# Kernel tuning notes

Measured on AMD Instinct MI355X. Metric: run time of the kernel, lower is better.

Reference implementation:

```python
import jax, jax.numpy as jnp
import numpy as np

N, E, T, Q, G = 50000, 800000, 1000000, 1000000, 4096
L, H, D, HID, ED = 3, 8, 16, 128, 16
EPS = 1e-8


def setup_inputs() -> dict:
    key = jax.random.key(0)
    ks = jax.random.split(key, 20)
    inp = {
        "x": jax.random.normal(ks[0], (N, HID), jnp.float32),
        "pos": jax.random.normal(ks[1], (N, 3), jnp.float32),
        "edge_attr": jax.random.normal(ks[2], (E, ED), jnp.float32),
        "temps": jax.random.uniform(ks[3], (G, 1), jnp.float32),
        "edge_index": jax.random.randint(ks[4], (2, E), 0, N, jnp.int32),
        "triple_index": jax.random.randint(ks[5], (3, T), 0, N, jnp.int32),
        "quadra_index": jax.random.randint(ks[6], (4, Q), 0, N, jnp.int32),
        "batch": jnp.sort(jax.random.randint(ks[7], (N,), 0, G, jnp.int32)),
        "W": jax.random.normal(ks[8], (L, HID, HID), jnp.float32) * 0.08,
        "a_e": jax.random.normal(ks[9], (L, H, 2 * D + 1), jnp.float32) * 0.1,
        "a_t": jax.random.normal(ks[10], (L, H, 2 * D + 1), jnp.float32) * 0.1,
        "a_q": jax.random.normal(ks[11], (L, H, 2 * D + 1), jnp.float32) * 0.1,
        "We": jax.random.normal(ks[12], (L, ED, H), jnp.float32) * 0.1,
        "W1": jax.random.normal(ks[13], (2 * HID + 1, 256), jnp.float32) * 0.06,
        "b1": jnp.zeros((256,), jnp.float32),
        "W2": jax.random.normal(ks[14], (256, 256), jnp.float32) * 0.06,
        "b2": jnp.zeros((256,), jnp.float32),
        "W3": jax.random.normal(ks[15], (256, 1), jnp.float32) * 0.06,
        "b3": jnp.zeros((1,), jnp.float32),
    }
    return inp


def _seg_softmax(logits, seg, n):
    # numerically stable segment softmax over destination nodes
    m = jax.ops.segment_max(logits, seg, num_segments=n)
    m = jnp.where(jnp.isfinite(m), m, 0.0)
    e = jnp.exp(logits - m[seg])
    s = jax.ops.segment_sum(e, seg, num_segments=n)
    return e / (s[seg] + 1e-16)


def _hop(hh, src, dst, geom, a, bias=None):
    # hh: [N,H,D]; gather-attend-scatter for one interaction order
    q, k = hh[dst], hh[src]                      # [M,H,D]
    logits = jnp.einsum('mhd,hd->mh', q, a[:, :D]) \
           + jnp.einsum('mhd,hd->mh', k, a[:, D:2 * D]) \
           + geom[:, None] * a[:, 2 * D]
    if bias is not None:
        logits = logits + bias
    logits = jax.nn.leaky_relu(logits, 0.2)
    alpha = _seg_softmax(logits, dst, hh.shape[0])  # [M,H]
    return jax.ops.segment_sum(k * alpha[..., None], dst, num_segments=hh.shape[0])


def _geom_features(pos, edge_index, triple_index, quadra_index):
    # edge distance
    d = jnp.linalg.norm(pos[edge_index[0]] - pos[edge_index[1]] + EPS, axis=-1)
    # triple angle cos at center node j of (i,j,k)
    i, j, k = triple_index
    u, v = pos[i] - pos[j], pos[k] - pos[j]
    cos_a = (u * v).sum(-1) / (jnp.linalg.norm(u, axis=-1) * jnp.linalg.norm(v, axis=-1) + EPS)
    # quadra dihedral cos of (p0,p1,p2,p3)
    p0, p1, p2, p3 = pos[quadra_index[0]], pos[quadra_index[1]], pos[quadra_index[2]], pos[quadra_index[3]]
    b1, b2, b3 = p1 - p0, p2 - p1, p3 - p2
    n1, n2 = jnp.cross(b1, b2), jnp.cross(b2, b3)
    cos_d = (n1 * n2).sum(-1) / (jnp.linalg.norm(n1, axis=-1) * jnp.linalg.norm(n2, axis=-1) + EPS)
    return d, cos_a, cos_d


def reference(x, pos, edge_attr, temps, edge_index, triple_index, quadra_index, batch,
              W, a_e, a_t, a_q, We, W1, b1, W2, b2, W3, b3):
    d, cos_a, cos_d = _geom_features(pos, edge_index, triple_index, quadra_index)
    e_src, e_dst = edge_index[1], edge_index[0]
    t_src, t_dst = triple_index[2], triple_index[0]
    q_src, q_dst = quadra_index[3], quadra_index[0]
    h = x
    for l in range(L):
        hl = h @ W[l]                              # [N,HID]
        hh = hl.reshape(N, H, D)
        bias_e = edge_attr @ We[l]                 # [E,H]
        agg = _hop(hh, e_src, e_dst, d, a_e[l], bias_e) \
            + _hop(hh, t_src, t_dst, cos_a, a_t[l]) \
            + _hop(hh, q_src, q_dst, cos_d, a_q[l])
        h = jax.nn.elu(hl + agg.reshape(N, HID))
    # readout: sum + max pooling per graph, concat temperature scalar
    s = jax.ops.segment_sum(h, batch, num_segments=G)
    mx = jax.ops.segment_max(h, batch, num_segments=G)
    mx = jnp.where(jnp.isfinite(mx), mx, 0.0)
    mol = jnp.concatenate([s, mx, temps], axis=-1)  # [G, 2*HID+1]
    hdn = jax.nn.elu(mol @ W1 + b1)
    hdn = jax.nn.elu(hdn @ W2 + b2)
    return hdn @ W3 + b3
```

## Files before the change

kernel.cpp:

```cpp
#include <hip/hip_runtime.h>
#include <hip/hip_fp16.h>

#define NN 50000
#define EE 800000
#define TT 1000000
#define QQ 1000000
#define GG 4096
#define HID 128
#define NH 8
#define DH 16
#define CAP 64

#define TILE 2048
#define KPT 8
#define NB 196
#define NBG 392

typedef unsigned int u32;
typedef unsigned int u32x4 __attribute__((ext_vector_type(4)));

__device__ __forceinline__ float eluf(float x){ return x > 0.f ? x : expm1f(x); }

__device__ __forceinline__ u32 pack_sg(int src, float g){
  return ((u32)src << 16) | (u32)__half_as_ushort(__float2half(g));
}

__global__ void k_count3(const int* __restrict__ ei, const int* __restrict__ ti, const int* __restrict__ qi,
                         int* __restrict__ cnt){
  int i = blockIdx.x*blockDim.x + threadIdx.x;
  if (i < EE) atomicAdd(&cnt[ei[i]], 1);
  else if (i < EE+TT) atomicAdd(&cnt[NN + ti[i-EE]], 1);
  else if (i < EE+TT+QQ) atomicAdd(&cnt[2*NN + qi[i-EE-TT]], 1);
}

__global__ __launch_bounds__(1024) void k_scan4(const int* __restrict__ cnt,
    int* __restrict__ off_e, int* __restrict__ off_t, int* __restrict__ off_q,
    int* __restrict__ cur_e, int* __restrict__ cur_t, int* __restrict__ cur_q,
    const int* __restrict__ batch, int* __restrict__ goff){
  int b = blockIdx.x, t = threadIdx.x;
  if (b == 3){
    for (int g=t; g<=GG; g+=1024){
      int lo=0, hi=NN;
      while (lo<hi){ int mid=(lo+hi)>>1; if (batch[mid]<g) lo=mid+1; else hi=mid; }
      goff[g]=lo;
    }
    return;
  }
  __shared__ int part[1024];
  const int* c = cnt + b*NN;
  int* off = (b==0)?off_e:(b==1)?off_t:off_q;
  int* cur = (b==0)?cur_e:(b==1)?cur_t:cur_q;
  int chunk = (NN + 1023) >> 10;
  int s0 = t*chunk, s1 = min(NN, s0+chunk);
  int sum = 0;
  for (int i=s0;i<s1;i++) sum += c[i];
  part[t] = sum;
  __syncthreads();
  for (int d=1; d<1024; d<<=1){
    int v = (t>=d) ? part[t-d] : 0;
    __syncthreads();
    part[t] += v;
    __syncthreads();
  }
  int run = (t==0) ? 0 : part[t-1];
  for (int i=s0;i<s1;i++){ off[i]=run; cur[i]=run; run += c[i]; }
  if (t==0) off[NN] = part[1023];
}

__global__ void k_fillE(const float* __restrict__ pos, const float* __restrict__ edge_attr,
    const int* __restrict__ ei, const float* __restrict__ We,
    int* __restrict__ cur_e, u32* __restrict__ eRec){
  int i = blockIdx.x*blockDim.x + threadIdx.x;
  if (i >= EE) return;
  int dn = ei[i], sn = ei[EE+i];
  float dx = pos[dn*3+0]-pos[sn*3+0]+1e-8f;
  float dy = pos[dn*3+1]-pos[sn*3+1]+1e-8f;
  float dz = pos[dn*3+2]-pos[sn*3+2]+1e-8f;
  float d = sqrtf(dx*dx+dy*dy+dz*dz);
  int p = atomicAdd(&cur_e[dn], 1);
  const float4* s = (const float4*)(edge_attr + (size_t)i*16);
  float4 v0=s[0], v1=s[1], v2=s[2], v3=s[3];
  float a[16] = {v0.x,v0.y,v0.z,v0.w, v1.x,v1.y,v1.z,v1.w,
                 v2.x,v2.y,v2.z,v2.w, v3.x,v3.y,v3.z,v3.w};
  u32x4 r[4];
  r[0][0] = pack_sg(sn, d); r[0][1]=0; r[0][2]=0; r[0][3]=0;
  #pragma unroll
  for (int l=0; l<3; l++){
    const float* Wel = We + l*DH*NH;
    #pragma unroll
    for (int hp=0; hp<4; hp++){
      float sa=0.f, sb=0.f;
      #pragma unroll
      for (int c=0;c<16;c++){
        sa = fmaf(a[c], Wel[c*NH + 2*hp],     sa);
        sb = fmaf(a[c], Wel[c*NH + 2*hp + 1], sb);
      }
      __half2 hh = __floats2half2_rn(sa, sb);
      r[1+l][hp] = *(u32*)&hh;
    }
  }
  u32x4* dst4 = (u32x4*)(eRec + (size_t)p*16);
  dst4[0]=r[0]; dst4[1]=r[1]; dst4[2]=r[2]; dst4[3]=r[3];
}

__global__ __launch_bounds__(256) void k_fillTQ_A(const float* __restrict__ pos,
    const int* __restrict__ ti, const int* __restrict__ qi,
    const int* __restrict__ off_t, const int* __restrict__ off_q,
    u32* __restrict__ gcur, uint2* __restrict__ stg){
  __shared__ u32 s_sg[TILE];
  __shared__ u32 s_dw[TILE];
  __shared__ u32 s_cnt[NBG];
  __shared__ u32 s_scan[512];
  __shared__ u32 s_gb[NBG];
  int t = threadIdx.x;
  size_t tile0 = (size_t)blockIdx.x * TILE;
  for (int i=t;i<NBG;i+=256) s_cnt[i]=0;
  __syncthreads();
  u32 my_sg[KPT], my_dw[KPT], my_rank[KPT]; int my_bg[KPT];
  #pragma unroll
  for (int k=0;k<KPT;k++){
    size_t idx = tile0 + (size_t)k*256 + t;
    my_bg[k] = -1;
    if (idx < (size_t)TT+QQ){
      int dst, src; float g;
      int typeq = (idx >= (size_t)TT);
      if (!typeq){
        int m = (int)idx;
        int ia=ti[m], jb=ti[TT+m], kc=ti[2*TT+m];
        float ux=pos[ia*3+0]-pos[jb*3+0], uy=pos[ia*3+1]-pos[jb*3+1], uz=pos[ia*3+2]-pos[jb*3+2];
        float vx=pos[kc*3+0]-pos[jb*3+0], vy=pos[kc*3+1]-pos[jb*3+1], vz=pos[kc*3+2]-pos[jb*3+2];
        float num = ux*vx+uy*vy+uz*vz;
        float den = sqrtf(ux*ux+uy*uy+uz*uz)*sqrtf(vx*vx+vy*vy+vz*vz) + 1e-8f;
        g = num/den; dst = ia; src = kc;
      } else {
        int m = (int)(idx - TT);
        int p0=qi[m], p1=qi[QQ+m], p2=qi[2*QQ+m], p3=qi[3*QQ+m];
        float b1x=pos[p1*3+0]-pos[p0*3+0], b1y=pos[p1*3+1]-pos[p0*3+1], b1z=pos[p1*3+2]-pos[p0*3+2];
        float b2x=pos[p2*3+0]-pos[p1*3+0], b2y=pos[p2*3+1]-pos[p1*3+1], b2z=pos[p2*3+2]-pos[p1*3+2];
        float b3x=pos[p3*3+0]-pos[p2*3+0], b3y=pos[p3*3+1]-pos[p2*3+1], b3z=pos[p3*3+2]-pos[p2*3+2];
        float n1x=b1y*b2z-b1z*b2y, n1y=b1z*b2x-b1x*b2z, n1z=b1x*b2y-b1y*b2x;
        float n2x=b2y*b3z-b2z*b3y, n2y=b2z*b3x-b2x*b3z, n2z=b2x*b3y-b2y*b3x;
        float num = n1x*n2x+n1y*n2y+n1z*n2z;
        float den = sqrtf(n1x*n1x+n1y*n1y+n1z*n1z)*sqrtf(n2x*n2x+n2y*n2y+n2z*n2z) + 1e-8f;
        g = num/den; dst = p0; src = p3;
      }
      int bg = (typeq?NB:0) + (dst>>8);
      my_sg[k] = pack_sg(src, g);
      my_dw[k] = (u32)dst | ((u32)typeq<<20);
      my_bg[k] = bg;
      my_rank[k] = atomicAdd(&s_cnt[bg], 1u);
    }
  }
  __syncthreads();
  int i0=t, i1=t+256;
  s_scan[i0] = (i0<NBG)? s_cnt[i0] : 0u;
  s_scan[i1] = (i1<NBG)? s_cnt[i1] : 0u;
  __syncthreads();
  for (int d=1; d<512; d<<=1){
    u32 a0 = (i0>=d)? s_scan[i0-d] : 0u;
    u32 a1 = (i1>=d)? s_scan[i1-d] : 0u;
    __syncthreads();
    s_scan[i0]+=a0; s_scan[i1]+=a1;
    __syncthreads();
  }
  u32 total = s_scan[NBG-1];
  #pragma unroll
  for (int k=0;k<KPT;k++){
    if (my_bg[k]>=0){
      u32 slot = s_scan[my_bg[k]] - s_cnt[my_bg[k]] + my_rank[k];
      s_sg[slot]=my_sg[k]; s_dw[slot]=my_dw[k];
    }
  }
  for (int i=t;i<NBG;i+=256)
    s_gb[i] = s_cnt[i] ? atomicAdd(&gcur[i], s_cnt[i]) : 0u;
  __syncthreads();
  for (u32 j=t; j<total; j+=256){
    u32 dw = s_dw[j];
    int typeq = (dw>>20)&1;
    int dst = dw & 0xFFFFF;
    int bg = (typeq?NB:0) + (dst>>8);
    u32 rank = j - (s_scan[bg]-s_cnt[bg]);
    int w0 = (typeq? bg-NB : bg)*256;
    size_t sbase = typeq ? (size_t)TT + (size_t)off_q[w0] : (size_t)off_t[w0];
    stg[sbase + s_gb[bg] + rank] = make_uint2(s_sg[j], dw);
  }
}

__global__ __launch_bounds__(256) void k_fillTQ_B(const uint2* __restrict__ stg,
    const int* __restrict__ off_t, const int* __restrict__ off_q,
    u32* __restrict__ csg_t, u32* __restrict__ csg_q){
  __shared__ int curL[256];
  int b = blockIdx.x, t = threadIdx.x;
  int typeq = (b>=NB);
  int bl = typeq? b-NB : b;
  const int* off = typeq? off_q : off_t;
  u32* csg = typeq? csg_q : csg_t;
  int w0 = bl*256, w1 = min(w0+256, NN);
  int s0 = off[w0], s1 = off[w1];
  for (int i=t; i<w1-w0; i+=256) curL[i] = off[w0+i];
  __syncthreads();
  size_t sb = (typeq? (size_t)TT : 0) + (size_t)s0;
  int cnt = s1 - s0;
  for (int i=t; i<cnt; i+=256){
    uint2 r = stg[sb+i];
    int dst = r.y & 0xFFFFF;
    int p = atomicAdd(&curL[dst-w0], 1);
    csg[p] = r.x;
  }
}

#define GR 16
__global__ __launch_bounds__(128) void k_gemm(const float* __restrict__ A, const float* __restrict__ W,
                                              __half* __restrict__ B16){
  int col = threadIdx.x;
  int r0 = blockIdx.x * GR;
  const float* Ab = A + (size_t)r0*HID;
  float acc[GR];
  #pragma unroll
  for (int r=0;r<GR;r++) acc[r]=0.f;
  #pragma unroll 4
  for (int k=0;k<HID;k++){
    float wv = W[k*HID+col];
    #pragma unroll
    for (int r=0;r<GR;r++) acc[r] = fmaf(Ab[r*HID+k], wv, acc[r]);
  }
  #pragma unroll
  for (int r=0;r<GR;r++) B16[(size_t)(r0+r)*HID+col] = __float2half(acc[r]);
}

__global__ void k_proj(const __half* __restrict__ hl16,
    const float* __restrict__ ae, const float* __restrict__ at, const float* __restrict__ aq,
    float* __restrict__ qa_e, float* __restrict__ ka_e,
    float* __restrict__ qa_t, float* __restrict__ ka_t,
    float* __restrict__ qa_q, float* __restrict__ ka_q){
  int i = blockIdx.x*blockDim.x + threadIdx.x;
  if (i >= NN*NH) return;
  int h = i & 7; int n = i >> 3;
  const __half2* v2 = (const __half2*)(hl16 + (size_t)n*HID + h*DH);
  float x[DH];
  #pragma unroll
  for (int d2=0; d2<8; d2++){ float2 f = __half22float2(v2[d2]); x[2*d2]=f.x; x[2*d2+1]=f.y; }
  const float* Ae = ae + h*33; const float* At_ = at + h*33; const float* Aq = aq + h*33;
  float s0=0,s1=0,s2=0,s3=0,s4=0,s5=0;
  #pragma unroll
  for (int d=0; d<DH; d++){
    s0 = fmaf(x[d], Ae[d],      s0);  s1 = fmaf(x[d], Ae[DH+d],  s1);
    s2 = fmaf(x[d], At_[d],     s2);  s3 = fmaf(x[d], At_[DH+d], s3);
    s4 = fmaf(x[d], Aq[d],      s4);  s5 = fmaf(x[d], Aq[DH+d],  s5);
  }
  qa_e[i]=s0; ka_e[i]=s1; qa_t[i]=s2; ka_t[i]=s3; qa_q[i]=s4; ka_q[i]=s5;
}

template<int EB>
__device__ __forceinline__ void hop_wave(
    int st, int deg, const u32* __restrict__ csg, const u32* __restrict__ eRec, int L4,
    const float* __restrict__ ka, const float* __restrict__ qa, const float* __restrict__ acoef,
    const __half* __restrict__ hh16, float* __restrict__ sa, int n, int l, int hg,
    float& o0, float& o1){
  float4 qv0 = *(const float4*)(qa + (size_t)n*8);
  float4 qv1 = *(const float4*)(qa + (size_t)n*8 + 4);
  float qa8[8] = {qv0.x,qv0.y,qv0.z,qv0.w,qv1.x,qv1.y,qv1.z,qv1.w};
  float cf[8];
  #pragma unroll
  for (int h=0;h<8;h++) cf[h] = acoef[h*33+32];
  float acc0=0.f, acc1=0.f, dsum=0.f;
  for (int base=0; base<deg; base+=CAP){
    int c = min(CAP, deg-base);
    u32 sg = 0;
    if (l < c){
      size_t idx = (size_t)(st+base+l);
      float bias8[8] = {0,0,0,0,0,0,0,0};
      if (EB){
        sg = eRec[idx*16];
        u32x4 br = *(const u32x4*)(eRec + idx*16 + 4 + L4);
        #pragma unroll
        for (int h=0;h<8;h++){
          u32 bw = br[h>>1];
          unsigned short us = (h&1)? (unsigned short)(bw>>16) : (unsigned short)(bw&0xFFFFu);
          bias8[h] = __half2float(__ushort_as_half(us));
        }
      } else {
        sg = csg[idx];
      }
      int src = (int)(sg>>16);
      float g = __half2float(__ushort_as_half((unsigned short)(sg&0xFFFFu)));
      float4 k0 = *(const float4*)(ka + (size_t)src*8);
      float4 k1 = *(const float4*)(ka + (size_t)src*8 + 4);
      float ka8[8] = {k0.x,k0.y,k0.z,k0.w,k1.x,k1.y,k1.z,k1.w};
      #pragma unroll
      for (int h=0;h<8;h++){
        float lg = qa8[h] + ka8[h] + g*cf[h] + bias8[h];
        lg = lg>=0.f ? lg : 0.2f*lg;
        sa[l*9+h] = __expf(lg);
      }
    }
    __builtin_amdgcn_wave_barrier();
    #pragma unroll 4
    for (int m=0; m<c; ++m){
      float am = sa[m*9+hg];
      u32 sv = __shfl(sg, m);
      int src = (int)(sv>>16);
      float2 f = __half22float2(*(const __half2*)&hh16[(size_t)src*HID + 2*l]);
      dsum += am;
      acc0 = fmaf(f.x, am, acc0);
      acc1 = fmaf(f.y, am, acc1);
    }
    __builtin_amdgcn_wave_barrier();
  }
  float inv = 1.f/(dsum + 1e-16f);
  o0 = fmaf(acc0, inv, o0);
  o1 = fmaf(acc1, inv, o1);
}

__global__ __launch_bounds__(256) void k_hop3(
    const int* __restrict__ off_e, const int* __restrict__ off_t, const int* __restrict__ off_q,
    const u32* __restrict__ eRec,
    const u32* __restrict__ csg_t, const u32* __restrict__ csg_q,
    const float* __restrict__ qa_e, const float* __restrict__ ka_e,
    const float* __restrict__ qa_t, const float* __restrict__ ka_t,
    const float* __restrict__ qa_q, const float* __restrict__ ka_q,
    const float* __restrict__ ae, const float* __restrict__ at, const float* __restrict__ aq,
    const __half* __restrict__ hh16, const __half* __restrict__ hlr16, float* __restrict__ hout,
    int L){
  __shared__ float sh_a[4][CAP*9];
  int t = threadIdx.x;
  int wv = t>>6, l = t&63;
  int n = blockIdx.x*4 + wv;
  if (n >= NN) return;
  float* sa = sh_a[wv];
  int hg = l>>3;
  float o0=0.f, o1=0.f;
  int se = off_e[n], de = off_e[n+1]-se;
  int st = off_t[n], dt = off_t[n+1]-st;
  int sq = off_q[n], dq = off_q[n+1]-sq;
  hop_wave<1>(se, de, nullptr, eRec, 4*L, ka_e, qa_e, ae, hh16, sa, n, l, hg, o0, o1);
  hop_wave<0>(st, dt, csg_t, nullptr, 0,  ka_t, qa_t, at, hh16, sa, n, l, hg, o0, o1);
  hop_wave<0>(sq, dq, csg_q, nullptr, 0,  ka_q, qa_q, aq, hh16, sa, n, l, hg, o0, o1);
  size_t oi = (size_t)n*HID + 2*l;
  float2 rf = __half22float2(*(const __half2*)&hlr16[oi]);
  *(float2*)&hout[oi] = make_float2(eluf(rf.x + o0), eluf(rf.y + o1));
}

__global__ __launch_bounds__(128) void k_pool(const float* __restrict__ h, const int* __restrict__ goff,
                                              float* __restrict__ gs, float* __restrict__ gmx){
  int g = blockIdx.x, t = threadIdx.x;
  int s = goff[g], e = goff[g+1];
  float sum = 0.f, mx = -INFINITY;
  for (int n=s; n<e; n++){
    float v = h[(size_t)n*HID+t];
    sum += v; mx = fmaxf(mx, v);
  }
  gs[(size_t)g*HID+t] = sum;
  gmx[(size_t)g*HID+t] = (s < e) ? mx : 0.f;
}

#define GPB 8
#define MSTR 260
__global__ __launch_bounds__(256) void k_mlp(const float* __restrict__ gs, const float* __restrict__ gmx,
    const float* __restrict__ temps,
    const float* __restrict__ W1, const float* __restrict__ b1,
    const float* __restrict__ W2, const float* __restrict__ b2,
    const float* __restrict__ W3, const float* __restrict__ b3,
    float* __restrict__ out){
  __shared__ float mol[GPB][MSTR];
  __shared__ float hd[GPB][MSTR];
  int g0 = blockIdx.x*GPB, t = threadIdx.x;
  for (int i=t; i<GPB*HID; i+=256){
    int g=i>>7, d=i&127;
    mol[g][d]     = gs[(size_t)(g0+g)*HID+d];
    mol[g][128+d] = gmx[(size_t)(g0+g)*HID+d];
  }
  if (t < GPB){ mol[t][256]=temps[g0+t]; mol[t][257]=0.f; mol[t][258]=0.f; mol[t][259]=0.f; }
  __syncthreads();
  float acc[GPB];
  #pragma unroll
  for (int g=0;g<GPB;g++) acc[g]=b1[t];
  for (int k0=0;k0<256;k0+=4){
    float w0=W1[(size_t)(k0+0)*256+t], w1=W1[(size_t)(k0+1)*256+t];
    float w2=W1[(size_t)(k0+2)*256+t], w3=W1[(size_t)(k0+3)*256+t];
    #pragma unroll
    for (int g=0;g<GPB;g++){
      float4 m4 = *(const float4*)&mol[g][k0];
      acc[g] = fmaf(m4.x,w0, fmaf(m4.y,w1, fmaf(m4.z,w2, fmaf(m4.w,w3, acc[g]))));
    }
  }
  { float wl=W1[(size_t)256*256+t];
    #pragma unroll
    for (int g=0;g<GPB;g++) acc[g]=fmaf(mol[g][256],wl,acc[g]); }
  #pragma unroll
  for (int g=0;g<GPB;g++) hd[g][t]=eluf(acc[g]);
  __syncthreads();
  #pragma unroll
  for (int g=0;g<GPB;g++) acc[g]=b2[t];
  for (int k0=0;k0<256;k0+=4){
    float w0=W2[(size_t)(k0+0)*256+t], w1=W2[(size_t)(k0+1)*256+t];
    float w2=W2[(size_t)(k0+2)*256+t], w3=W2[(size_t)(k0+3)*256+t];
    #pragma unroll
    for (int g=0;g<GPB;g++){
      float4 h4 = *(const float4*)&hd[g][k0];
      acc[g] = fmaf(h4.x,w0, fmaf(h4.y,w1, fmaf(h4.z,w2, fmaf(h4.w,w3, acc[g]))));
    }
  }
  float w3v = W3[t];
  #pragma unroll
  for (int g=0;g<GPB;g++) mol[g][t] = eluf(acc[g])*w3v;
  __syncthreads();
  int g = t >> 5, j = t & 31;
  float s = 0.f;
  for (int i=j; i<256; i+=32) s += mol[g][i];
  #pragma unroll
  for (int d=16; d>0; d>>=1) s += __shfl_down(s, d, 32);
  if (j == 0) out[g0+g] = s + b3[0];
}

extern "C" void kernel_launch(void* const* d_in, const int* in_sizes, int n_in,
                              void* d_out, int out_size, void* d_ws, size_t ws_size,
                              hipStream_t stream){
  const float* x         = (const float*)d_in[0];
  const float* pos       = (const float*)d_in[1];
  const float* edge_attr = (const float*)d_in[2];
  const float* temps     = (const float*)d_in[3];
  const int*   ei        = (const int*)d_in[4];
  const int*   ti        = (const int*)d_in[5];
  const int*   qi        = (const int*)d_in[6];
  const int*   batch     = (const int*)d_in[7];
  const float* W         = (const float*)d_in[8];
  const float* a_e       = (const float*)d_in[9];
  const float* a_t       = (const float*)d_in[10];
  const float* a_q       = (const float*)d_in[11];
  const float* We        = (const float*)d_in[12];
  const float* W1        = (const float*)d_in[13];
  const float* b1        = (const float*)d_in[14];
  const float* W2        = (const float*)d_in[15];
  const float* b2        = (const float*)d_in[16];
  const float* W3        = (const float*)d_in[17];
  const float* b3        = (const float*)d_in[18];
  float* out = (float*)d_out;

  char* base = (char*)d_ws; size_t woff = 0;
  auto alloc = [&](size_t bytes)->void*{
    void* p = base + woff;
    woff = (woff + bytes + 255) & ~(size_t)255;
    return p;
  };
  float*  hbuf   = (float*)alloc((size_t)NN*HID*4);
  __half* hl16   = (__half*)alloc((size_t)NN*HID*2);
  float*  qa_e   = (float*)alloc((size_t)NN*NH*4);
  float*  ka_e   = (float*)alloc((size_t)NN*NH*4);
  float*  qa_t   = (float*)alloc((size_t)NN*NH*4);
  float*  ka_t   = (float*)alloc((size_t)NN*NH*4);
  float*  qa_q   = (float*)alloc((size_t)NN*NH*4);
  float*  ka_q   = (float*)alloc((size_t)NN*NH*4);
  u32*    eRec   = (u32*)alloc((size_t)EE*64);
  u32*    csg_t  = (u32*)alloc((size_t)TT*4);
  u32*    csg_q  = (u32*)alloc((size_t)QQ*4);
  uint2*  stg    = (uint2*)alloc((size_t)(TT+QQ)*8);
  float*  gs     = (float*)alloc((size_t)GG*HID*4);
  float*  gmx    = (float*)alloc((size_t)GG*HID*4);
  int*    cnt    = (int*)alloc((size_t)3*NN*4);
  u32*    gcur   = (u32*)alloc((size_t)NBG*4);
  int*    off_e  = (int*)alloc((size_t)(NN+1)*4);
  int*    off_t  = (int*)alloc((size_t)(NN+1)*4);
  int*    off_q  = (int*)alloc((size_t)(NN+1)*4);
  int*    cur_e  = (int*)alloc((size_t)NN*4);
  int*    cur_t  = (int*)alloc((size_t)NN*4);
  int*    cur_q  = (int*)alloc((size_t)NN*4);
  int*    goff   = (int*)alloc((size_t)(GG+1)*4);

  hipMemsetAsync(cnt, 0, (size_t)3*NN*4, stream);
  hipMemsetAsync(gcur, 0, (size_t)NBG*4, stream);
  int tot = EE+TT+QQ;
  k_count3<<<(tot+255)/256,256,0,stream>>>(ei, ti, qi, cnt);
  k_scan4<<<4,1024,0,stream>>>(cnt, off_e, off_t, off_q, cur_e, cur_t, cur_q, batch, goff);
  k_fillE<<<(EE+255)/256,256,0,stream>>>(pos, edge_attr, ei, We, cur_e, eRec);
  k_fillTQ_A<<<(TT+QQ+TILE-1)/TILE,256,0,stream>>>(pos, ti, qi, off_t, off_q, gcur, stg);
  k_fillTQ_B<<<NBG,256,0,stream>>>(stg, off_t, off_q, csg_t, csg_q);

  for (int l=0; l<3; l++){
    const float* hin = (l==0) ? x : hbuf;
    k_gemm<<<NN/GR,128,0,stream>>>(hin, W + (size_t)l*HID*HID, hl16);
    k_proj<<<(NN*NH+255)/256,256,0,stream>>>(hl16, a_e+l*264, a_t+l*264, a_q+l*264,
                                             qa_e, ka_e, qa_t, ka_t, qa_q, ka_q);
    k_hop3<<<(NN+3)/4,256,0,stream>>>(off_e, off_t, off_q, eRec, csg_t, csg_q,
                                      qa_e, ka_e, qa_t, ka_t, qa_q, ka_q,
                                      a_e+l*264, a_t+l*264, a_q+l*264,
                                      hl16, hl16, hbuf, l);
  }

  k_pool<<<GG,128,0,stream>>>(hbuf, goff, gs, gmx);
  k_mlp<<<GG/GPB,256,0,stream>>>(gs, gmx, temps, W1, b1, W2, b2, W3, b3, out);
}
```

Measured before the change: 1.184 ms.

## Fuse attention projection into GEMM, merge three hops into one persistent pass

The per-head q/k attention projections are now computed inside the GEMM kernel from an LDS tile, which removes the separate projection kernel. The projections are stored as fp16 to halve gather traffic. The hop kernel becomes a grid-stride persistent kernel. It processes edge, triple and quad neighbours in the same chunk loop, storing fp16-packed attention weights and source ids in per-wave LDS slots, so the three gathers can overlap. The costs are extra fp16 rounding of the logits and weights, and load imbalance if the degree distributions differ.

New measurement: 1.064 ms. 10.1% less time.

```diff
diff --git a/kernel.cpp b/kernel.cpp
--- a/kernel.cpp
+++ b/kernel.cpp
@@ -10,6 +10,7 @@
 #define NH 8
 #define DH 16
 #define CAP 64
+#define SLOT 5
 
 #define TILE 2048
 #define KPT 8
@@ -23,6 +24,17 @@
 
 __device__ __forceinline__ u32 pack_sg(int src, float g){
   return ((u32)src << 16) | (u32)__half_as_ushort(__float2half(g));
+}
+__device__ __forceinline__ float lo16(u32 w){ return __half2float(__ushort_as_half((unsigned short)(w&0xFFFFu))); }
+__device__ __forceinline__ float hi16(u32 w){ return __half2float(__ushort_as_half((unsigned short)(w>>16))); }
+__device__ __forceinline__ u32 packf2(float a, float b){
+  __half2 h = __floats2half2_rn(a,b);
+  return *(u32*)&h;
+}
+__device__ __forceinline__ void unpack8(const __half* p, float* o){
+  u32x4 w = *(const u32x4*)p;
+  #pragma unroll
+  for (int j=0;j<4;j++){ u32 x=w[j]; o[2*j]=lo16(x); o[2*j+1]=hi16(x); }
 }
 
 __global__ void k_count3(const int* __restrict__ ei, const int* __restrict__ ti, const int* __restrict__ qi,
@@ -95,8 +107,7 @@
         sa = fmaf(a[c], Wel[c*NH + 2*hp],     sa);
         sb = fmaf(a[c], Wel[c*NH + 2*hp + 1], sb);
       }
-      __half2 hh = __floats2half2_rn(sa, sb);
-      r[1+l][hp] = *(u32*)&hh;
+      r[1+l][hp] = packf2(sa, sb);
     }
   }
   u32x4* dst4 = (u32x4*)(eRec + (size_t)p*16);
@@ -210,8 +221,13 @@
 }
 
 #define GR 16
-__global__ __launch_bounds__(128) void k_gemm(const float* __restrict__ A, const float* __restrict__ W,
-                                              __half* __restrict__ B16){
+__global__ __launch_bounds__(128) void k_gemm(const float* __restrict__ A, const float* __restrict__ Wm,
+    const float* __restrict__ ae, const float* __restrict__ at, const float* __restrict__ aq,
+    __half* __restrict__ B16,
+    __half* __restrict__ qa_e, __half* __restrict__ ka_e,
+    __half* __restrict__ qa_t, __half* __restrict__ ka_t,
+    __half* __restrict__ qa_q, __half* __restrict__ ka_q){
+  __shared__ float sh[GR][132];
   int col = threadIdx.x;
   int r0 = blockIdx.x * GR;
   const float* Ab = A + (size_t)r0*HID;
@@ -220,26 +236,20 @@
   for (int r=0;r<GR;r++) acc[r]=0.f;
   #pragma unroll 4
   for (int k=0;k<HID;k++){
-    float wv = W[k*HID+col];
+    float wv = Wm[k*HID+col];
     #pragma unroll
     for (int r=0;r<GR;r++) acc[r] = fmaf(Ab[r*HID+k], wv, acc[r]);
   }
   #pragma unroll
-  for (int r=0;r<GR;r++) B16[(size_t)(r0+r)*HID+col] = __float2half(acc[r]);
-}
-
-__global__ void k_proj(const __half* __restrict__ hl16,
-    const float* __restrict__ ae, const float* __restrict__ at, const float* __restrict__ aq,
-    float* __restrict__ qa_e, float* __restrict__ ka_e,
-    float* __restrict__ qa_t, float* __restrict__ ka_t,
-    float* __restrict__ qa_q, float* __restrict__ ka_q){
-  int i = blockIdx.x*blockDim.x + threadIdx.x;
-  if (i >= NN*NH) return;
-  int h = i & 7; int n = i >> 3;
-  const __half2* v2 = (const __half2*)(hl16 + (size_t)n*HID + h*DH);
+  for (int r=0;r<GR;r++){
+    B16[(size_t)(r0+r)*HID+col] = __float2half(acc[r]);
+    sh[r][col] = acc[r];
+  }
+  __syncthreads();
+  int r = threadIdx.x>>3, h = threadIdx.x&7;
   float x[DH];
   #pragma unroll
-  for (int d2=0; d2<8; d2++){ float2 f = __half22float2(v2[d2]); x[2*d2]=f.x; x[2*d2+1]=f.y; }
+  for (int j=0;j<DH;j++) x[j] = sh[r][h*DH+j];
   const float* Ae = ae + h*33; const float* At_ = at + h*33; const float* Aq = aq + h*33;
   float s0=0,s1=0,s2=0,s3=0,s4=0,s5=0;
   #pragma unroll
@@ -248,97 +258,140 @@
     s2 = fmaf(x[d], At_[d],     s2);  s3 = fmaf(x[d], At_[DH+d], s3);
     s4 = fmaf(x[d], Aq[d],      s4);  s5 = fmaf(x[d], Aq[DH+d],  s5);
   }
-  qa_e[i]=s0; ka_e[i]=s1; qa_t[i]=s2; ka_t[i]=s3; qa_q[i]=s4; ka_q[i]=s5;
-}
-
-template<int EB>
-__device__ __forceinline__ void hop_wave(
-    int st, int deg, const u32* __restrict__ csg, const u32* __restrict__ eRec, int L4,
-    const float* __restrict__ ka, const float* __restrict__ qa, const float* __restrict__ acoef,
-    const __half* __restrict__ hh16, float* __restrict__ sa, int n, int l, int hg,
-    float& o0, float& o1){
-  float4 qv0 = *(const float4*)(qa + (size_t)n*8);
-  float4 qv1 = *(const float4*)(qa + (size_t)n*8 + 4);
-  float qa8[8] = {qv0.x,qv0.y,qv0.z,qv0.w,qv1.x,qv1.y,qv1.z,qv1.w};
-  float cf[8];
-  #pragma unroll
-  for (int h=0;h<8;h++) cf[h] = acoef[h*33+32];
-  float acc0=0.f, acc1=0.f, dsum=0.f;
-  for (int base=0; base<deg; base+=CAP){
-    int c = min(CAP, deg-base);
-    u32 sg = 0;
-    if (l < c){
-      size_t idx = (size_t)(st+base+l);
-      float bias8[8] = {0,0,0,0,0,0,0,0};
-      if (EB){
-        sg = eRec[idx*16];
-        u32x4 br = *(const u32x4*)(eRec + idx*16 + 4 + L4);
-        #pragma unroll
-        for (int h=0;h<8;h++){
-          u32 bw = br[h>>1];
-          unsigned short us = (h&1)? (unsigned short)(bw>>16) : (unsigned short)(bw&0xFFFFu);
-          bias8[h] = __half2float(__ushort_as_half(us));
-        }
-      } else {
-        sg = csg[idx];
-      }
-      int src = (int)(sg>>16);
-      float g = __half2float(__ushort_as_half((unsigned short)(sg&0xFFFFu)));
-      float4 k0 = *(const float4*)(ka + (size_t)src*8);
-      float4 k1 = *(const float4*)(ka + (size_t)src*8 + 4);
-      float ka8[8] = {k0.x,k0.y,k0.z,k0.w,k1.x,k1.y,k1.z,k1.w};
-      #pragma unroll
-      for (int h=0;h<8;h++){
-        float lg = qa8[h] + ka8[h] + g*cf[h] + bias8[h];
-        lg = lg>=0.f ? lg : 0.2f*lg;
-        sa[l*9+h] = __expf(lg);
-      }
-    }
-    __builtin_amdgcn_wave_barrier();
-    #pragma unroll 4
-    for (int m=0; m<c; ++m){
-      float am = sa[m*9+hg];
-      u32 sv = __shfl(sg, m);
-      int src = (int)(sv>>16);
-      float2 f = __half22float2(*(const __half2*)&hh16[(size_t)src*HID + 2*l]);
-      dsum += am;
-      acc0 = fmaf(f.x, am, acc0);
-      acc1 = fmaf(f.y, am, acc1);
-    }
-    __builtin_amdgcn_wave_barrier();
-  }
-  float inv = 1.f/(dsum + 1e-16f);
-  o0 = fmaf(acc0, inv, o0);
-  o1 = fmaf(acc1, inv, o1);
+  size_t o = (size_t)(r0+r)*NH + h;
+  qa_e[o]=__float2half(s0); ka_e[o]=__float2half(s1);
+  qa_t[o]=__float2half(s2); ka_t[o]=__float2half(s3);
+  qa_q[o]=__float2half(s4); ka_q[o]=__float2half(s5);
 }
 
 __global__ __launch_bounds__(256) void k_hop3(
     const int* __restrict__ off_e, const int* __restrict__ off_t, const int* __restrict__ off_q,
     const u32* __restrict__ eRec,
     const u32* __restrict__ csg_t, const u32* __restrict__ csg_q,
-    const float* __restrict__ qa_e, const float* __restrict__ ka_e,
-    const float* __restrict__ qa_t, const float* __restrict__ ka_t,
-    const float* __restrict__ qa_q, const float* __restrict__ ka_q,
+    const __half* __restrict__ qa_e, const __half* __restrict__ ka_e,
+    const __half* __restrict__ qa_t, const __half* __restrict__ ka_t,
+    const __half* __restrict__ qa_q, const __half* __restrict__ ka_q,
     const float* __restrict__ ae, const float* __restrict__ at, const float* __restrict__ aq,
     const __half* __restrict__ hh16, const __half* __restrict__ hlr16, float* __restrict__ hout,
-    int L){
-  __shared__ float sh_a[4][CAP*9];
+    int L, int nwaves){
+  __shared__ u32 sw[4][3*CAP*SLOT];
   int t = threadIdx.x;
   int wv = t>>6, l = t&63;
-  int n = blockIdx.x*4 + wv;
-  if (n >= NN) return;
-  float* sa = sh_a[wv];
+  u32* Wb = sw[wv];
   int hg = l>>3;
-  float o0=0.f, o1=0.f;
-  int se = off_e[n], de = off_e[n+1]-se;
-  int st = off_t[n], dt = off_t[n+1]-st;
-  int sq = off_q[n], dq = off_q[n+1]-sq;
-  hop_wave<1>(se, de, nullptr, eRec, 4*L, ka_e, qa_e, ae, hh16, sa, n, l, hg, o0, o1);
-  hop_wave<0>(st, dt, csg_t, nullptr, 0,  ka_t, qa_t, at, hh16, sa, n, l, hg, o0, o1);
-  hop_wave<0>(sq, dq, csg_q, nullptr, 0,  ka_q, qa_q, aq, hh16, sa, n, l, hg, o0, o1);
-  size_t oi = (size_t)n*HID + 2*l;
-  float2 rf = __half22float2(*(const __half2*)&hlr16[oi]);
-  *(float2*)&hout[oi] = make_float2(eluf(rf.x + o0), eluf(rf.y + o1));
+  int wi = hg>>1, shft = (hg&1)*16;
+  float cfE[8], cfT[8], cfQ[8];
+  #pragma unroll
+  for (int h=0;h<8;h++){ cfE[h]=ae[h*33+32]; cfT[h]=at[h*33+32]; cfQ[h]=aq[h*33+32]; }
+  for (int n = blockIdx.x*4 + wv; n < NN; n += nwaves){
+    int se=off_e[n], de=off_e[n+1]-se;
+    int st=off_t[n], dt=off_t[n+1]-st;
+    int sq=off_q[n], dq=off_q[n+1]-sq;
+    float aE0=0,aE1=0,aT0=0,aT1=0,aQ0=0,aQ1=0,dE=0,dT=0,dQ=0;
+    int maxd = max(de, max(dt, dq));
+    for (int base=0; base<maxd; base+=CAP){
+      int ce = min(CAP, de-base); if (ce<0) ce=0;
+      int ct = min(CAP, dt-base); if (ct<0) ct=0;
+      int cq = min(CAP, dq-base); if (cq<0) cq=0;
+      if (l < ce){
+        size_t idx = (size_t)(se+base+l);
+        u32 sg = eRec[idx*16];
+        u32x4 br = *(const u32x4*)(eRec + idx*16 + 4 + 4*L);
+        int src = (int)(sg>>16);
+        float g = lo16(sg);
+        float ka8[8]; unpack8(ka_e + (size_t)src*NH, ka8);
+        float qa8[8]; unpack8(qa_e + (size_t)n*NH, qa8);
+        u32* sl = Wb + l*SLOT;
+        #pragma unroll
+        for (int j=0;j<4;j++){
+          u32 bw = br[j];
+          float l0 = qa8[2*j]   + ka8[2*j]   + g*cfE[2*j]   + lo16(bw);
+          float l1 = qa8[2*j+1] + ka8[2*j+1] + g*cfE[2*j+1] + hi16(bw);
+          l0 = l0>=0.f ? l0 : 0.2f*l0;
+          l1 = l1>=0.f ? l1 : 0.2f*l1;
+          sl[j] = packf2(__expf(l0), __expf(l1));
+        }
+        sl[4] = (u32)src;
+      }
+      if (l < ct){
+        u32 sg = csg_t[(size_t)(st+base+l)];
+        int src = (int)(sg>>16);
+        float g = lo16(sg);
+        float ka8[8]; unpack8(ka_t + (size_t)src*NH, ka8);
+        float qa8[8]; unpack8(qa_t + (size_t)n*NH, qa8);
+        u32* sl = Wb + CAP*SLOT + l*SLOT;
+        #pragma unroll
+        for (int j=0;j<4;j++){
+          float l0 = qa8[2*j]   + ka8[2*j]   + g*cfT[2*j];
+          float l1 = qa8[2*j+1] + ka8[2*j+1] + g*cfT[2*j+1];
+          l0 = l0>=0.f ? l0 : 0.2f*l0;
+          l1 = l1>=0.f ? l1 : 0.2f*l1;
+          sl[j] = packf2(__expf(l0), __expf(l1));
+        }
+        sl[4] = (u32)src;
+      }
+      if (l < cq){
+        u32 sg = csg_q[(size_t)(sq+base+l)];
+        int src = (int)(sg>>16);
+        float g = lo16(sg);
+        float ka8[8]; unpack8(ka_q + (size_t)src*NH, ka8);
+        float qa8[8]; unpack8(qa_q + (size_t)n*NH, qa8);
+        u32* sl = Wb + 2*CAP*SLOT + l*SLOT;
+        #pragma unroll
+        for (int j=0;j<4;j++){
+          float l0 = qa8[2*j]   + ka8[2*j]   + g*cfQ[2*j];
+          float l1 = qa8[2*j+1] + ka8[2*j+1] + g*cfQ[2*j+1];
+          l0 = l0>=0.f ? l0 : 0.2f*l0;
+          l1 = l1>=0.f ? l1 : 0.2f*l1;
+          sl[j] = packf2(__expf(l0), __expf(l1));
+        }
+        sl[4] = (u32)src;
+      }
+      __builtin_amdgcn_wave_barrier();
+      {
+        const u32* P = Wb;
+        #pragma unroll 4
+        for (int m=0;m<ce;m++){
+          u32 aw = P[m*SLOT+wi];
+          u32 sr = P[m*SLOT+4];
+          float am = __half2float(__ushort_as_half((unsigned short)(aw>>shft)));
+          float2 f = __half22float2(*((const __half2*)(hh16 + (size_t)sr*HID) + l));
+          dE += am; aE0 = fmaf(f.x, am, aE0); aE1 = fmaf(f.y, am, aE1);
+        }
+      }
+      {
+        const u32* P = Wb + CAP*SLOT;
+        #pragma unroll 4
+        for (int m=0;m<ct;m++){
+          u32 aw = P[m*SLOT+wi];
+          u32 sr = P[m*SLOT+4];
+          float am = __half2float(__ushort_as_half((unsigned short)(aw>>shft)));
+          float2 f = __half22float2(*((const __half2*)(hh16 + (size_t)sr*HID) + l));
+          dT += am; aT0 = fmaf(f.x, am, aT0); aT1 = fmaf(f.y, am, aT1);
+        }
+      }
+      {
+        const u32* P = Wb + 2*CAP*SLOT;
+        #pragma unroll 4
+        for (int m=0;m<cq;m++){
+          u32 aw = P[m*SLOT+wi];
+          u32 sr = P[m*SLOT+4];
+          float am = __half2float(__ushort_as_half((unsigned short)(aw>>shft)));
+          float2 f = __half22float2(*((const __half2*)(hh16 + (size_t)sr*HID) + l));
+          dQ += am; aQ0 = fmaf(f.x, am, aQ0); aQ1 = fmaf(f.y, am, aQ1);
+        }
+      }
+      __builtin_amdgcn_wave_barrier();
+    }
+    float invE = 1.f/(dE + 1e-16f);
+    float invT = 1.f/(dT + 1e-16f);
+    float invQ = 1.f/(dQ + 1e-16f);
+    float o0 = aE0*invE + aT0*invT + aQ0*invQ;
+    float o1 = aE1*invE + aT1*invT + aQ1*invQ;
+    size_t oi = (size_t)n*HID + 2*l;
+    float2 rf = __half22float2(*(const __half2*)&hlr16[oi]);
+    *(float2*)&hout[oi] = make_float2(eluf(rf.x + o0), eluf(rf.y + o1));
+  }
 }
 
 __global__ __launch_bounds__(128) void k_pool(const float* __restrict__ h, const int* __restrict__ goff,
@@ -445,12 +498,12 @@
   };
   float*  hbuf   = (float*)alloc((size_t)NN*HID*4);
   __half* hl16   = (__half*)alloc((size_t)NN*HID*2);
-  float*  qa_e   = (float*)alloc((size_t)NN*NH*4);
-  float*  ka_e   = (float*)alloc((size_t)NN*NH*4);
-  float*  qa_t   = (float*)alloc((size_t)NN*NH*4);
-  float*  ka_t   = (float*)alloc((size_t)NN*NH*4);
-  float*  qa_q   = (float*)alloc((size_t)NN*NH*4);
-  float*  ka_q   = (float*)alloc((size_t)NN*NH*4);
+  __half* qa_e   = (__half*)alloc((size_t)NN*NH*2);
+  __half* ka_e   = (__half*)alloc((size_t)NN*NH*2);
+  __half* qa_t   = (__half*)alloc((size_t)NN*NH*2);
+  __half* ka_t   = (__half*)alloc((size_t)NN*NH*2);
+  __half* qa_q   = (__half*)alloc((size_t)NN*NH*2);
+  __half* ka_q   = (__half*)alloc((size_t)NN*NH*2);
   u32*    eRec   = (u32*)alloc((size_t)EE*64);
   u32*    csg_t  = (u32*)alloc((size_t)TT*4);
   u32*    csg_q  = (u32*)alloc((size_t)QQ*4);
@@ -476,15 +529,17 @@
   k_fillTQ_A<<<(TT+QQ+TILE-1)/TILE,256,0,stream>>>(pos, ti, qi, off_t, off_q, gcur, stg);
   k_fillTQ_B<<<NBG,256,0,stream>>>(stg, off_t, off_q, csg_t, csg_q);
 
+  int hopBlocks = 2048;
+  int nwaves = hopBlocks*4;
   for (int l=0; l<3; l++){
     const float* hin = (l==0) ? x : hbuf;
-    k_gemm<<<NN/GR,128,0,stream>>>(hin, W + (size_t)l*HID*HID, hl16);
-    k_proj<<<(NN*NH+255)/256,256,0,stream>>>(hl16, a_e+l*264, a_t+l*264, a_q+l*264,
-                                             qa_e, ka_e, qa_t, ka_t, qa_q, ka_q);
-    k_hop3<<<(NN+3)/4,256,0,stream>>>(off_e, off_t, off_q, eRec, csg_t, csg_q,
-                                      qa_e, ka_e, qa_t, ka_t, qa_q, ka_q,
-                                      a_e+l*264, a_t+l*264, a_q+l*264,
-                                      hl16, hl16, hbuf, l);
+    k_gemm<<<NN/GR,128,0,stream>>>(hin, W + (size_t)l*HID*HID,
+                                   a_e+l*264, a_t+l*264, a_q+l*264,
+                                   hl16, qa_e, ka_e, qa_t, ka_t, qa_q, ka_q);
+    k_hop3<<<hopBlocks,256,0,stream>>>(off_e, off_t, off_q, eRec, csg_t, csg_q,
+                                       qa_e, ka_e, qa_t, ka_t, qa_q, ka_q,
+                                       a_e+l*264, a_t+l*264, a_q+l*264,
+                                       hl16, hl16, hbuf, l, nwaves);
   }
 
   k_pool<<<GG,128,0,stream>>>(hbuf, goff, gs, gmx);
```
